# Kernel tuning notes

Hardware: AMD Instinct MI355X
Metric: run time of the kernel (lower is better)

Reference implementation:

```python
import jax, jax.numpy as jnp
import numpy as np

B, CIN, COUT, N, S, K, KS, DIM = 4, 64, 64, 32768, 8192, 32, 16, 3


def setup_inputs() -> dict:
    key = jax.random.key(0)
    ks = jax.random.split(key, 9)
    x = jax.random.normal(ks[0], (B, CIN, N), dtype=jnp.float32)
    pos = jax.random.normal(ks[1], (B, DIM, N), dtype=jnp.float32)
    support_points = jax.random.normal(ks[2], (B, DIM, S), dtype=jnp.float32)
    neighbors_indices = jax.random.randint(ks[3], (B, S, K), 0, N, dtype=jnp.int64)
    radius = jnp.ones((1,), dtype=jnp.float32)
    # learned params (Conv2d with 1x1 kernels == per-point matmuls)
    w_fc1 = jax.random.normal(ks[4], (KS, DIM), dtype=jnp.float32) * 0.1   # fc1: dim -> kernel_size
    w_fc2 = jax.random.normal(ks[5], (KS, 2 * KS), dtype=jnp.float32) * 0.1
    w_fc3 = jax.random.normal(ks[6], (KS, 2 * KS), dtype=jnp.float32) * 0.1
    w_cv = jax.random.normal(ks[7], (COUT, CIN, KS), dtype=jnp.float32) * 0.05  # Conv2d(CIN,COUT,(1,KS))
    return {"x": x, "pos": pos, "support_points": support_points,
            "neighbors_indices": neighbors_indices, "radius": radius,
            "w_fc1": w_fc1, "w_fc2": w_fc2, "w_fc3": w_fc3, "w_cv": w_cv}


def _gather(feat, idx):
    # feat: [B, C, N], idx: [B, S, K] -> [B, C, S, K]
    return jax.vmap(lambda f, i: f[:, i])(feat, idx)


def reference(x, pos, support_points, neighbors_indices, radius,
              w_fc1, w_fc2, w_fc3, w_cv):
    mask = (neighbors_indices > -1)                       # [B,S,K]
    idx = jnp.where(mask, neighbors_indices, 0)
    pos_g = _gather(pos, idx)                             # [B,3,S,K]
    x_g = _gather(x, idx)                                 # [B,CIN,S,K]

    pts = pos_g - support_points[..., None]               # [B,3,S,K]
    mask_pts = (~jnp.isinf(pts[:, :1])).astype(pts.dtype) # [B,1,S,K]
    pts = jnp.nan_to_num(pts, nan=0.0, posinf=0.0, neginf=0.0)
    pts = pts / radius[0]

    # distance weight: L2-normalize binary mask over neighbor axis (torch F.normalize, eps=1e-12)
    mf = mask.astype(pts.dtype)                           # [B,S,K]
    nrm = jnp.sqrt(jnp.sum(mf * mf, axis=2, keepdims=True))
    dw = (mf / jnp.maximum(nrm, 1e-12))[:, None]          # [B,1,S,K]
    dw = dw * mask_pts

    mat = jax.nn.relu(jnp.einsum('kd,bdsn->bksn', w_fc1, pts)) * dw
    mp1 = jnp.max(mat, axis=3, keepdims=True)
    mat = jnp.concatenate([mat, jnp.broadcast_to(mp1, mat.shape)], axis=1)
    mat = jax.nn.relu(jnp.einsum('km,bmsn->bksn', w_fc2, mat)) * dw
    mp2 = jnp.max(mat, axis=3, keepdims=True)
    mat = jnp.concatenate([mat, jnp.broadcast_to(mp2, mat.shape)], axis=1)
    mat = jax.nn.relu(jnp.einsum('km,bmsn->bksn', w_fc3, mat)) * dw    # [B,KS,S,K]

    # features[b,s,c,k] = sum_n x_g[b,c,s,n] * mat[b,k,s,n]
    feats = jnp.einsum('bcsn,bksn->bcsk', x_g, mat)        # [B,CIN,S,KS]
    out = jnp.einsum('ock,bcsk->bos', w_cv, feats)         # [B,COUT,S]

    sup_inf = jnp.isinf(support_points[:, :1, :])          # [B,1,S]
    out = jnp.where(sup_inf, jnp.inf, out)
    return out
```

## Files before the change

### kernel.cpp

```cpp
#include <hip/hip_runtime.h>
#include <math.h>

#define B_    4
#define CIN_  64
#define COUT_ 64
#define N_    32768
#define S_    8192

typedef __attribute__((ext_vector_type(8))) short short8;
typedef __attribute__((ext_vector_type(4))) float f32x4a;

static __device__ __forceinline__ unsigned short f2bf(float x) {
    unsigned u = __float_as_uint(x);
    u += 0x7fffu + ((u >> 16) & 1u);
    return (unsigned short)(u >> 16);
}
static __device__ __forceinline__ unsigned pack2bf(float a, float b) {
    return (unsigned)f2bf(a) | ((unsigned)f2bf(b) << 16);
}
template <int CTRL>
static __device__ __forceinline__ float max_ror(float v) {
    float r = __int_as_float(__builtin_amdgcn_update_dpp(
        __float_as_int(v), __float_as_int(v), CTRL, 0xf, 0xf, false));
    return fmaxf(v, r);
}
#define ROR8 0x128
#define ROR4 0x124
#define ROR2 0x122
#define ROR1 0x121

static __device__ __forceinline__ int fl(int p, int col) {
    return p * 2048 + (col ^ ((p & 7) << 4) ^ (((col >> 7) & 3) << 5));
}

__global__ __launch_bounds__(256) void transpose_x_kernel(
    const float* __restrict__ x, unsigned short* __restrict__ xTB)
{
    __shared__ float tile[64][65];
    const int b  = blockIdx.y;
    const int n0 = blockIdx.x * 64;
    const int tx = threadIdx.x & 63;
    const int ty = threadIdx.x >> 6;

    const float* xb = x + (size_t)b * CIN_ * N_;
    #pragma unroll
    for (int c = ty; c < 64; c += 4)
        tile[c][tx] = xb[(size_t)c * N_ + n0 + tx];
    __syncthreads();

    const int cp = threadIdx.x & 31;
    const int r0 = threadIdx.x >> 5;
    unsigned short* xTb = xTB + ((size_t)b * N_ + n0) * 64;
    #pragma unroll
    for (int nn = r0; nn < 64; nn += 8) {
        ushort2 v;
        v.x = f2bf(tile[2 * cp][nn]);
        v.y = f2bf(tile[2 * cp + 1][nn]);
        *(ushort2*)&xTb[(size_t)nn * 64 + 2 * cp] = v;
    }
}

__global__ __launch_bounds__(256) void post_kernel(
    const float* __restrict__ pos, float* __restrict__ posT)
{
    const int b = blockIdx.y;
    const int n = blockIdx.x * 256 + threadIdx.x;
    const float* pb = pos + (size_t)b * 3 * N_;
    float4 v = make_float4(pb[n], pb[N_ + n], pb[2 * N_ + n], 0.0f);
    *(float4*)&posT[((size_t)b * N_ + n) * 4] = v;
}

__global__ __launch_bounds__(256) void wcvb_kernel(
    const float* __restrict__ wcv, unsigned short* __restrict__ wcvB)
{
    const int i = blockIdx.x * 256 + threadIdx.x;
    const int o   = i >> 10;
    const int rem = i & 1023;
    const int k   = rem >> 6;
    const int c   = rem & 63;
    wcvB[i] = f2bf(wcv[(size_t)o * 1024 + c * 16 + k]);
}

__global__ __launch_bounds__(512) void fka_fused_kernel(
    const float* __restrict__ posT, const float* __restrict__ sup,
    const int*   __restrict__ nbr, const float* __restrict__ radius,
    const float* __restrict__ w1,  const float* __restrict__ w2,
    const float* __restrict__ w3,  const unsigned short* __restrict__ xTB,
    const unsigned short* __restrict__ wcvB,
    float* __restrict__ out)
{
    __shared__ unsigned short featsL[16 * 1024];
    __shared__ int   idxs[16][32];
    __shared__ float t2s[16][16];
    __shared__ float pbuf[1024];

    const int b  = blockIdx.y;
    const int t  = threadIdx.x;
    const int g  = t >> 5;
    const int n  = t & 31;
    const int s0 = blockIdx.x * 16;
    const int s  = s0 + g;

    const int raw    = nbr[(((size_t)b * S_ + s) << 5) + n];
    const bool valid = raw > -1;
    const int id     = valid ? raw : 0;

    unsigned long long bal = __ballot(valid);
    unsigned bits = (unsigned)(bal >> (t & 32));
    const float nrm = sqrtf((float)__popc(bits));
    float dw = valid ? (1.0f / fmaxf(nrm, 1e-12f)) : 0.0f;

    const float4 pg = *(const float4*)&posT[((size_t)b * N_ + id) * 4];
    float px = pg.x - sup[(size_t)(b * 3 + 0) * S_ + s];
    float py = pg.y - sup[(size_t)(b * 3 + 1) * S_ + s];
    float pz = pg.z - sup[(size_t)(b * 3 + 2) * S_ + s];
    if (isinf(px)) dw = 0.0f;
    px = (isnan(px) || isinf(px)) ? 0.0f : px;
    py = (isnan(py) || isinf(py)) ? 0.0f : py;
    pz = (isnan(pz) || isinf(pz)) ? 0.0f : pz;
    const float inv_r = 1.0f / radius[0];
    px *= inv_r; py *= inv_r; pz *= inv_r;

    const int kk = n & 15;

    float m1[16], mp1[16], m2[16], mp2[16], m3[16];

    #pragma unroll
    for (int k = 0; k < 16; ++k) {
        float v = w1[k * 3 + 0] * px + w1[k * 3 + 1] * py + w1[k * 3 + 2] * pz;
        m1[k] = fmaxf(v, 0.0f) * dw;
    }
    #pragma unroll
    for (int k = 0; k < 16; ++k) {
        float v = m1[k];
        v = fmaxf(v, __shfl_xor(v, 16, 32));
        v = max_ror<ROR8>(v); v = max_ror<ROR4>(v);
        v = max_ror<ROR2>(v); v = max_ror<ROR1>(v);
        mp1[k] = v;
    }
    {
        const float* wb = &w2[kk * 32 + 16];
        float pa = 0.0f, pb = 0.0f;
        #pragma unroll
        for (int j = 0; j < 8; ++j) pa = fmaf(wb[j], mp1[j], pa);
        #pragma unroll
        for (int j = 0; j < 8; ++j) pb = fmaf(wb[8 + j], mp1[8 + j], pb);
        float tp = (n & 16) ? pb : pa;
        tp += __shfl_xor(tp, 16, 32);
        t2s[g][kk] = tp;
    }
    {
        float4 ta = *(const float4*)&t2s[g][0];
        float4 tb = *(const float4*)&t2s[g][4];
        float4 tc = *(const float4*)&t2s[g][8];
        float4 td = *(const float4*)&t2s[g][12];
        float t2v[16] = {ta.x, ta.y, ta.z, ta.w, tb.x, tb.y, tb.z, tb.w,
                         tc.x, tc.y, tc.z, tc.w, td.x, td.y, td.z, td.w};
        #pragma unroll
        for (int k = 0; k < 16; ++k) {
            const float* wr = &w2[k * 32];
            float v = t2v[k];
            #pragma unroll
            for (int j = 0; j < 16; ++j) v = fmaf(wr[j], m1[j], v);
            m2[k] = fmaxf(v, 0.0f) * dw;
        }
    }
    #pragma unroll
    for (int k = 0; k < 16; ++k) {
        float v = m2[k];
        v = fmaxf(v, __shfl_xor(v, 16, 32));
        v = max_ror<ROR8>(v); v = max_ror<ROR4>(v);
        v = max_ror<ROR2>(v); v = max_ror<ROR1>(v);
        mp2[k] = v;
    }
    {
        const float* wb = &w3[kk * 32 + 16];
        float pa = 0.0f, pb = 0.0f;
        #pragma unroll
        for (int j = 0; j < 8; ++j) pa = fmaf(wb[j], mp2[j], pa);
        #pragma unroll
        for (int j = 0; j < 8; ++j) pb = fmaf(wb[8 + j], mp2[8 + j], pb);
        float tp = (n & 16) ? pb : pa;
        tp += __shfl_xor(tp, 16, 32);
        t2s[g][kk] = tp;
    }
    {
        float4 ta = *(const float4*)&t2s[g][0];
        float4 tb = *(const float4*)&t2s[g][4];
        float4 tc = *(const float4*)&t2s[g][8];
        float4 td = *(const float4*)&t2s[g][12];
        float t3v[16] = {ta.x, ta.y, ta.z, ta.w, tb.x, tb.y, tb.z, tb.w,
                         tc.x, tc.y, tc.z, tc.w, td.x, td.y, td.z, td.w};
        #pragma unroll
        for (int k = 0; k < 16; ++k) {
            const float* wr = &w3[k * 32];
            float v = t3v[k];
            #pragma unroll
            for (int j = 0; j < 16; ++j) v = fmaf(wr[j], m2[j], v);
            m3[k] = fmaxf(v, 0.0f) * dw;
        }
    }

    idxs[g][n] = id;
    {
        const int hi = n >> 3, jj = n & 7;
        unsigned short* base = &featsL[g * 1024 + hi * 128 + jj];
        #pragma unroll
        for (int k = 0; k < 16; ++k) {
            const int row = (k + hi + g) & 15;
            base[row * 8] = f2bf(m3[k]);
        }
    }

    const int wv  = t >> 6;
    const int l   = t & 63;
    const int hi2 = l >> 4;
    const int k15 = l & 15;
    const unsigned short* xb = xTB + (size_t)b * N_ * 64;
    char* fLp = (char*)featsL;

    short8 bfrag[2];
    #pragma unroll
    for (int pp = 0; pp < 2; ++pp) {
        const int p = wv * 2 + pp;
        const int brow = (k15 + hi2 + p) & 15;
        bfrag[pp] = *(const short8*)&featsL[p * 1024 + hi2 * 128 + brow * 8];
    }

    #pragma unroll
    for (int pp = 0; pp < 2; ++pp) {
        const int p = wv * 2 + pp;

        int ids8[8];
        #pragma unroll
        for (int j = 0; j < 8; ++j) ids8[j] = idxs[p][hi2 * 8 + j];

        f32x4a acc[4];
        #pragma unroll
        for (int ct = 0; ct < 4; ++ct) acc[ct] = (f32x4a){0.f, 0.f, 0.f, 0.f};

        #pragma unroll
        for (int ct = 0; ct < 4; ++ct) {
            union { unsigned short u[8]; short8 v; } A;
            #pragma unroll
            for (int j = 0; j < 8; ++j)
                A.u[j] = xb[((size_t)ids8[j] << 6) + ct * 16 + k15];
            acc[ct] = __builtin_amdgcn_mfma_f32_16x16x32_bf16(A.v, bfrag[pp], acc[ct], 0, 0, 0);
        }

        #pragma unroll
        for (int ct = 0; ct < 4; ++ct) {
            uint2 val;
            val.x = pack2bf(acc[ct][0], acc[ct][1]);
            val.y = pack2bf(acc[ct][2], acc[ct][3]);
            const int col = k15 * 128 + ct * 32 + hi2 * 8;
            *(uint2*)(fLp + fl(p, col)) = val;
        }
    }
    __syncthreads();

    const int ot  = wv & 3;
    const int kh  = wv >> 2;
    const int lq  = hi2;
    const int l15 = k15;

    const unsigned short* apod =
        wcvB + (size_t)(ot * 16 + l15) * 1024 + kh * 512 + lq * 8;

    f32x4a oacc = (f32x4a){0.f, 0.f, 0.f, 0.f};
    #pragma unroll 4
    for (int ks = 0; ks < 16; ++ks) {
        const int col = kh * 1024 + ks * 64 + lq * 16;
        short8 bfv = *(const short8*)(fLp + fl(l15, col));
        short8 afv = *(const short8*)(apod + ks * 32);
        oacc = __builtin_amdgcn_mfma_f32_16x16x32_bf16(afv, bfv, oacc, 0, 0, 0);
    }

    if (kh == 1) {
        #pragma unroll
        for (int r = 0; r < 4; ++r)
            pbuf[ot * 256 + (lq * 4 + r) * 16 + l15] = oacc[r];
    }
    __syncthreads();
    if (kh == 0) {
        const int sidx = s0 + l15;
        const bool infs = isinf(sup[(size_t)b * 3 * S_ + sidx]);
        #pragma unroll
        for (int r = 0; r < 4; ++r) {
            const float v = oacc[r] + pbuf[ot * 256 + (lq * 4 + r) * 16 + l15];
            const int o = ot * 16 + lq * 4 + r;
            out[((size_t)b * COUT_ + o) * S_ + sidx] = infs ? INFINITY : v;
        }
    }
}

extern "C" void kernel_launch(void* const* d_in, const int* in_sizes, int n_in,
                              void* d_out, int out_size, void* d_ws, size_t ws_size,
                              hipStream_t stream)
{
    const float* x   = (const float*)d_in[0];
    const float* pos = (const float*)d_in[1];
    const float* sup = (const float*)d_in[2];
    const int*   nbr = (const int*)d_in[3];
    const float* rad = (const float*)d_in[4];
    const float* w1  = (const float*)d_in[5];
    const float* w2  = (const float*)d_in[6];
    const float* w3  = (const float*)d_in[7];
    const float* wcv = (const float*)d_in[8];
    float* out = (float*)d_out;

    char* p = (char*)d_ws;
    unsigned short* xTB = (unsigned short*)p;  p += (size_t)B_ * N_ * 64 * sizeof(unsigned short);
    float* posT = (float*)p;                   p += (size_t)B_ * N_ * 4 * sizeof(float);
    unsigned short* wcvB = (unsigned short*)p; p += (size_t)COUT_ * 1024 * sizeof(unsigned short);

    transpose_x_kernel<<<dim3(N_ / 64, B_), 256, 0, stream>>>(x, xTB);
    post_kernel<<<dim3(N_ / 256, B_), 256, 0, stream>>>(pos, posT);
    wcvb_kernel<<<dim3(256), 256, 0, stream>>>(wcv, wcvB);

    fka_fused_kernel<<<dim3(S_ / 16, B_), 512, 0, stream>>>(
        posT, sup, nbr, rad, w1, w2, w3, xTB, wcvB, out);
}
```

Baseline: 80.65 us.

## Prefetch gathered x rows early and pass neighbor ids via wave shuffles

Neighbor indices are now distributed with wave-level shuffles instead of a shared-memory idxs array. The gather of bf16 x rows for the first group is issued before the fc2/fc3 MLP math, and the second group's gather is issued before the first MFMA, so global-load latency overlaps compute. The w2/w3 weight rows used for the max-pool term are also loaded into registers once, up front. In exchange, register pressure rises from 64 extra prefetched shorts per thread, which may lower occupancy at 512 threads per block.

```diff
diff --git a/kernel.cpp b/kernel.cpp
--- a/kernel.cpp
+++ b/kernel.cpp
@@ -90,7 +90,6 @@
     float* __restrict__ out)
 {
     __shared__ unsigned short featsL[16 * 1024];
-    __shared__ int   idxs[16][32];
     __shared__ float t2s[16][16];
     __shared__ float pbuf[1024];
 
@@ -100,6 +99,10 @@
     const int n  = t & 31;
     const int s0 = blockIdx.x * 16;
     const int s  = s0 + g;
+    const int wv = t >> 6;
+    const int l  = t & 63;
+    const int hi2 = l >> 4;
+    const int k15 = l & 15;
 
     const int raw    = nbr[(((size_t)b * S_ + s) << 5) + n];
     const bool valid = raw > -1;
@@ -109,6 +112,13 @@
     unsigned bits = (unsigned)(bal >> (t & 32));
     const float nrm = sqrtf((float)__popc(bits));
     float dw = valid ? (1.0f / fmaxf(nrm, 1e-12f)) : 0.0f;
+
+    int ids0[8], ids1[8];
+    #pragma unroll
+    for (int j = 0; j < 8; ++j) {
+        ids0[j] = __shfl(id, hi2 * 8 + j, 64);
+        ids1[j] = __shfl(id, 32 + hi2 * 8 + j, 64);
+    }
 
     const float4 pg = *(const float4*)&posT[((size_t)b * N_ + id) * 4];
     float px = pg.x - sup[(size_t)(b * 3 + 0) * S_ + s];
@@ -122,6 +132,7 @@
     px *= inv_r; py *= inv_r; pz *= inv_r;
 
     const int kk = n & 15;
+    const unsigned short* xb = xTB + (size_t)b * N_ * 64;
 
     float m1[16], mp1[16], m2[16], mp2[16], m3[16];
 
@@ -138,17 +149,36 @@
         v = max_ror<ROR2>(v); v = max_ror<ROR1>(v);
         mp1[k] = v;
     }
-    {
-        const float* wb = &w2[kk * 32 + 16];
+
+    float wb2r[16], wb3r[16];
+    {
+        const float* wp2 = &w2[kk * 32 + 16];
+        const float* wp3 = &w3[kk * 32 + 16];
+        #pragma unroll
+        for (int q = 0; q < 4; ++q) {
+            *(float4*)&wb2r[q * 4] = *(const float4*)&wp2[q * 4];
+            *(float4*)&wb3r[q * 4] = *(const float4*)&wp3[q * 4];
+        }
+    }
+
+    {
         float pa = 0.0f, pb = 0.0f;
         #pragma unroll
-        for (int j = 0; j < 8; ++j) pa = fmaf(wb[j], mp1[j], pa);
-        #pragma unroll
-        for (int j = 0; j < 8; ++j) pb = fmaf(wb[8 + j], mp1[8 + j], pb);
+        for (int j = 0; j < 8; ++j) pa = fmaf(wb2r[j], mp1[j], pa);
+        #pragma unroll
+        for (int j = 0; j < 8; ++j) pb = fmaf(wb2r[8 + j], mp1[8 + j], pb);
         float tp = (n & 16) ? pb : pa;
         tp += __shfl_xor(tp, 16, 32);
         t2s[g][kk] = tp;
     }
+
+    unsigned short xp0[4][8];
+    #pragma unroll
+    for (int ct = 0; ct < 4; ++ct)
+        #pragma unroll
+        for (int j = 0; j < 8; ++j)
+            xp0[ct][j] = xb[((size_t)ids0[j] << 6) + ct * 16 + k15];
+
     {
         float4 ta = *(const float4*)&t2s[g][0];
         float4 tb = *(const float4*)&t2s[g][4];
@@ -174,12 +204,11 @@
         mp2[k] = v;
     }
     {
-        const float* wb = &w3[kk * 32 + 16];
         float pa = 0.0f, pb = 0.0f;
         #pragma unroll
-        for (int j = 0; j < 8; ++j) pa = fmaf(wb[j], mp2[j], pa);
-        #pragma unroll
-        for (int j = 0; j < 8; ++j) pb = fmaf(wb[8 + j], mp2[8 + j], pb);
+        for (int j = 0; j < 8; ++j) pa = fmaf(wb3r[j], mp2[j], pa);
+        #pragma unroll
+        for (int j = 0; j < 8; ++j) pb = fmaf(wb3r[8 + j], mp2[8 + j], pb);
         float tp = (n & 16) ? pb : pa;
         tp += __shfl_xor(tp, 16, 32);
         t2s[g][kk] = tp;
@@ -201,7 +230,6 @@
         }
     }
 
-    idxs[g][n] = id;
     {
         const int hi = n >> 3, jj = n & 7;
         unsigned short* base = &featsL[g * 1024 + hi * 128 + jj];
@@ -212,11 +240,6 @@
         }
     }
 
-    const int wv  = t >> 6;
-    const int l   = t & 63;
-    const int hi2 = l >> 4;
-    const int k15 = l & 15;
-    const unsigned short* xb = xTB + (size_t)b * N_ * 64;
     char* fLp = (char*)featsL;
 
     short8 bfrag[2];
@@ -227,32 +250,41 @@
         bfrag[pp] = *(const short8*)&featsL[p * 1024 + hi2 * 128 + brow * 8];
     }
 
-    #pragma unroll
-    for (int pp = 0; pp < 2; ++pp) {
-        const int p = wv * 2 + pp;
-
-        int ids8[8];
-        #pragma unroll
-        for (int j = 0; j < 8; ++j) ids8[j] = idxs[p][hi2 * 8 + j];
-
-        f32x4a acc[4];
-        #pragma unroll
-        for (int ct = 0; ct < 4; ++ct) acc[ct] = (f32x4a){0.f, 0.f, 0.f, 0.f};
-
+    unsigned short xp1[4][8];
+    #pragma unroll
+    for (int ct = 0; ct < 4; ++ct)
+        #pragma unroll
+        for (int j = 0; j < 8; ++j)
+            xp1[ct][j] = xb[((size_t)ids1[j] << 6) + ct * 16 + k15];
+
+    {
+        const int p = wv * 2;
         #pragma unroll
         for (int ct = 0; ct < 4; ++ct) {
             union { unsigned short u[8]; short8 v; } A;
             #pragma unroll
-            for (int j = 0; j < 8; ++j)
-                A.u[j] = xb[((size_t)ids8[j] << 6) + ct * 16 + k15];
-            acc[ct] = __builtin_amdgcn_mfma_f32_16x16x32_bf16(A.v, bfrag[pp], acc[ct], 0, 0, 0);
-        }
-
+            for (int j = 0; j < 8; ++j) A.u[j] = xp0[ct][j];
+            f32x4a acc = (f32x4a){0.f, 0.f, 0.f, 0.f};
+            acc = __builtin_amdgcn_mfma_f32_16x16x32_bf16(A.v, bfrag[0], acc, 0, 0, 0);
+            uint2 val;
+            val.x = pack2bf(acc[0], acc[1]);
+            val.y = pack2bf(acc[2], acc[3]);
+            const int col = k15 * 128 + ct * 32 + hi2 * 8;
+            *(uint2*)(fLp + fl(p, col)) = val;
+        }
+    }
+    {
+        const int p = wv * 2 + 1;
         #pragma unroll
         for (int ct = 0; ct < 4; ++ct) {
+            union { unsigned short u[8]; short8 v; } A;
+            #pragma unroll
+            for (int j = 0; j < 8; ++j) A.u[j] = xp1[ct][j];
+            f32x4a acc = (f32x4a){0.f, 0.f, 0.f, 0.f};
+            acc = __builtin_amdgcn_mfma_f32_16x16x32_bf16(A.v, bfrag[1], acc, 0, 0, 0);
             uint2 val;
-            val.x = pack2bf(acc[ct][0], acc[ct][1]);
-            val.y = pack2bf(acc[ct][2], acc[ct][3]);
+            val.x = pack2bf(acc[0], acc[1]);
+            val.y = pack2bf(acc[2], acc[3]);
             const int col = k15 * 128 + ct * 32 + hi2 * 8;
             *(uint2*)(fLp + fl(p, col)) = val;
         }
```

Measured after the change: 82.74 us. 2.6% more time.
